# Kernel optimization log

Hardware: AMD Instinct MI355X
Metric: run time of the kernel (lower is better)

Reference implementation:

```python
import jax, jax.numpy as jnp
import numpy as np


def setup_inputs() -> dict:
    key = jax.random.key(0)
    k1, k2, k3, k4, k5 = jax.random.split(key, 5)
    B, T, D, H = 128, 512, 128, 512
    x = jax.random.normal(k1, (B, T, D), dtype=jnp.float32)
    h = jnp.zeros((B, H), dtype=jnp.float32)
    # tau in [1, 2) so the Euler step h + (-h + upd)/tau is stable
    tau = jax.random.uniform(k2, (B, 1), dtype=jnp.float32) + 1.0
    s_in = 1.0 / np.sqrt(D)
    s_rec = 1.0 / np.sqrt(H)
    # torch nn.Linear default init: U(-1/sqrt(fan_in), 1/sqrt(fan_in))
    W_in_w = jax.random.uniform(k3, (H, D), dtype=jnp.float32, minval=-s_in, maxval=s_in)
    W_in_b = jax.random.uniform(k4, (H,), dtype=jnp.float32, minval=-s_in, maxval=s_in)
    W_rec_w = jax.random.uniform(k5, (H, H), dtype=jnp.float32, minval=-s_rec, maxval=s_rec)
    return {"x": x, "h": h, "tau": tau, "W_in_w": W_in_w, "W_in_b": W_in_b, "W_rec_w": W_rec_w}


def reference(x, h, tau, W_in_w, W_in_b, W_rec_w):
    # Precompute the input projection for all timesteps in one big GEMM.
    # x: [B,T,D], W_in_w: [H,D] -> x_in: [B,T,H]
    x_in = jnp.einsum('btd,hd->bth', x, W_in_w) + W_in_b

    def step(h_t, xin_t):
        # xin_t: [B,H]; recurrent GEMM + tanh + Euler update (true data dep on h_t)
        upd = jnp.tanh(xin_t + h_t @ W_rec_w.T)
        h_new = h_t + (-h_t + upd) / tau
        return h_new, h_new

    h_last, h_seq = jax.lax.scan(step, h, jnp.swapaxes(x_in, 0, 1))  # scan over T
    return jnp.swapaxes(h_seq, 0, 1), h_last  # ([B,T,H], [B,H])
```

## Files before the change

### kernel.cpp

```cpp
#include <hip/hip_runtime.h>

#define B_SZ 128
#define T_SZ 512
#define D_SZ 128
#define H_SZ 512

#define NG 8
#define GB 16
#define NS 4
#define SN 128

typedef _Float16 f16;
typedef _Float16 f16x8 __attribute__((ext_vector_type(8)));
typedef _Float16 f16x4 __attribute__((ext_vector_type(4)));
typedef float f32x4 __attribute__((ext_vector_type(4)));
typedef unsigned long long ull;

__global__ __launch_bounds__(256) void transpose_k(const float* __restrict__ in,
                                                   float* __restrict__ out,
                                                   int R, int C) {
  __shared__ float tile[32][33];
  int c0 = blockIdx.x * 32, r0 = blockIdx.y * 32;
  int tx = threadIdx.x & 31, ty = threadIdx.x >> 5;
  for (int i = ty; i < 32; i += 8)
    tile[i][tx] = in[(size_t)(r0 + i) * C + (c0 + tx)];
  __syncthreads();
  for (int i = ty; i < 32; i += 8)
    out[(size_t)(c0 + i) * R + (r0 + tx)] = tile[tx][i];
}

__global__ __launch_bounds__(256) void input_proj_k(
    const float* __restrict__ x,
    const float* __restrict__ WTin,
    const float* __restrict__ bias,
    float* __restrict__ out)
{
  __shared__ float xs[32 * 128];
  const int tid = threadIdx.x;
  const size_t r0 = (size_t)blockIdx.x * 32;

  const float4* xg = (const float4*)(x + r0 * D_SZ);
  float4* xs4s = (float4*)xs;
#pragma unroll
  for (int i = 0; i < 4; ++i) xs4s[tid + i * 256] = xg[tid + i * 256];
  __syncthreads();

  const int q = tid & 127;
  const int rg = tid >> 7;
  const float4* W4 = (const float4*)WTin;
  const float4* xs4 = (const float4*)xs;

  float acc[16][4];
#pragma unroll
  for (int r = 0; r < 16; ++r)
#pragma unroll
    for (int c = 0; c < 4; ++c) acc[r][c] = 0.f;

  for (int k4 = 0; k4 < 32; ++k4) {
    float w[4][4];
#pragma unroll
    for (int kk = 0; kk < 4; ++kk) {
      float4 wv = W4[(size_t)(k4 * 4 + kk) * 128 + q];
      w[kk][0] = wv.x; w[kk][1] = wv.y; w[kk][2] = wv.z; w[kk][3] = wv.w;
    }
#pragma unroll
    for (int r = 0; r < 16; ++r) {
      float4 xv = xs4[(rg * 16 + r) * 32 + k4];
      float xk[4] = {xv.x, xv.y, xv.z, xv.w};
#pragma unroll
      for (int kk = 0; kk < 4; ++kk)
#pragma unroll
        for (int c = 0; c < 4; ++c)
          acc[r][c] = fmaf(xk[kk], w[kk][c], acc[r][c]);
    }
  }

  float4 bv = ((const float4*)bias)[q];
  float bb[4] = {bv.x, bv.y, bv.z, bv.w};
#pragma unroll
  for (int r = 0; r < 16; ++r) {
    float4 o;
    o.x = acc[r][0] + bb[0];
    o.y = acc[r][1] + bb[1];
    o.z = acc[r][2] + bb[2];
    o.w = acc[r][3] + bb[3];
    ((float4*)(out + (r0 + rg * 16 + r) * H_SZ))[q] = o;
  }
}

__device__ __forceinline__ float fast_tanh(float y) {
  float e = __expf(2.0f * y);
  return 1.0f - __fdividef(2.0f, e + 1.0f);
}

__device__ __forceinline__ ull ld_agent(const ull* p) {
  return __hip_atomic_load(p, __ATOMIC_RELAXED, __HIP_MEMORY_SCOPE_AGENT);
}

__global__ __launch_bounds__(512) void ltc_rec_mfma(
    float* __restrict__ seq,
    float* __restrict__ h_last,
    const float* __restrict__ hin,
    const float* __restrict__ tau,
    const float* __restrict__ Wrec,
    f16* __restrict__ ex)
{
  __shared__ f16 hs[2][GB * H_SZ];

  const int tid = threadIdx.x;
  const int g = blockIdx.x & 7;
  const int slice = blockIdx.x >> 3;
  const int w = tid >> 6;
  const int l = tid & 63;
  const int m = l & 15;
  const int kg = l >> 4;
  const int jt = slice * SN + w * 16;
  const int j0 = jt + kg * 4;
  const int b = g * GB + m;

  f16x8 afrag[16];
  {
    const float* wr = Wrec + (size_t)(jt + m) * H_SZ;
#pragma unroll
    for (int ff = 0; ff < 16; ++ff) {
      const int f = (slice * 4 + ff) & 15;
      const int k0 = f * 32 + kg * 8;
      float4 u0 = *(const float4*)(wr + k0);
      float4 u1 = *(const float4*)(wr + k0 + 4);
      f16x8 a;
      a[0] = (f16)u0.x; a[1] = (f16)u0.y; a[2] = (f16)u0.z; a[3] = (f16)u0.w;
      a[4] = (f16)u1.x; a[5] = (f16)u1.y; a[6] = (f16)u1.z; a[7] = (f16)u1.w;
      afrag[ff] = a;
    }
  }

  float hreg[4];
  {
    float4 h0 = *(const float4*)(hin + (size_t)b * H_SZ + j0);
    hreg[0] = h0.x; hreg[1] = h0.y; hreg[2] = h0.z; hreg[3] = h0.w;
  }
  const float itau = 1.0f / tau[b];

  {
    const int mr = tid >> 5;
    const int c4 = (tid & 31) * 4;
#pragma unroll
    for (int p = 0; p < 4; ++p) {
      const int col = p * SN + c4;
      float4 v = *(const float4*)(hin + (size_t)(g * GB + mr) * H_SZ + col);
      const int e = (mr * H_SZ + col) ^ ((mr & 7) << 3);
      f16x4 hf;
      hf[0] = (f16)v.x; hf[1] = (f16)v.y; hf[2] = (f16)v.z; hf[3] = (f16)v.w;
      *(f16x4*)&hs[0][e] = hf;
    }
  }
  __syncthreads();

  const size_t EXB = (size_t)GB * SN;
  const size_t RING_ULL = (size_t)NG * NS * EXB / 4;
  ull* pub0 = (ull*)(ex + ((size_t)g * NS + slice) * EXB + (size_t)m * SN + (w * 16 + kg * 4));

  const int gmr = tid >> 5;
  const int gc4 = (tid & 31) * 4;
  const int psa = (slice + 1) & 3, psb = (slice + 2) & 3, psc = (slice + 3) & 3;
  const ull* ga0 = (const ull*)(ex + ((size_t)g * NS + psa) * EXB + (size_t)gmr * SN + gc4);
  const ull* gb0 = (const ull*)(ex + ((size_t)g * NS + psb) * EXB + (size_t)gmr * SN + gc4);
  const ull* gc0 = (const ull*)(ex + ((size_t)g * NS + psc) * EXB + (size_t)gmr * SN + gc4);
  const int ea = (gmr * H_SZ + psa * SN + gc4) ^ ((gmr & 7) << 3);
  const int eb = (gmr * H_SZ + psb * SN + gc4) ^ ((gmr & 7) << 3);
  const int ec = (gmr * H_SZ + psc * SN + gc4) ^ ((gmr & 7) << 3);
  const int eown = (m * H_SZ + j0) ^ ((m & 7) << 3);

  int ebase[16];
#pragma unroll
  for (int ff = 0; ff < 16; ++ff) {
    const int f = (slice * 4 + ff) & 15;
    ebase[ff] = (m * H_SZ + f * 32 + kg * 8) ^ ((m & 7) << 3);
  }

  float* seqp = seq + (size_t)b * T_SZ * H_SZ + j0;
  float4 xin = *(const float4*)seqp;

  for (int s = 0; s < T_SZ; ++s) {
    const int cur = s & 1, nxt = cur ^ 1;

    ull w0 = 0, w1 = 0, w2 = 0;
    const size_t proff = nxt ? RING_ULL : 0;
    const ull ptag = (ull)(((s - 1) >> 1) & 1);
    if (s > 0) {
      w0 = ld_agent(ga0 + proff);
      w1 = ld_agent(gb0 + proff);
      w2 = ld_agent(gc0 + proff);
    }

    f32x4 accA = {0.f, 0.f, 0.f, 0.f};
    accA = __builtin_amdgcn_mfma_f32_16x16x32_f16(afrag[0], *(const f16x8*)&hs[cur][ebase[0]], accA, 0, 0, 0);
    accA = __builtin_amdgcn_mfma_f32_16x16x32_f16(afrag[1], *(const f16x8*)&hs[cur][ebase[1]], accA, 0, 0, 0);
    accA = __builtin_amdgcn_mfma_f32_16x16x32_f16(afrag[2], *(const f16x8*)&hs[cur][ebase[2]], accA, 0, 0, 0);
    accA = __builtin_amdgcn_mfma_f32_16x16x32_f16(afrag[3], *(const f16x8*)&hs[cur][ebase[3]], accA, 0, 0, 0);

    if (s > 0) {
      while ((w0 & 1ULL) != ptag) w0 = ld_agent(ga0 + proff);
      while ((w1 & 1ULL) != ptag) w1 = ld_agent(gb0 + proff);
      while ((w2 & 1ULL) != ptag) w2 = ld_agent(gc0 + proff);
      *(f16x4*)&hs[cur][ea] = __builtin_bit_cast(f16x4, w0);
      *(f16x4*)&hs[cur][eb] = __builtin_bit_cast(f16x4, w1);
      *(f16x4*)&hs[cur][ec] = __builtin_bit_cast(f16x4, w2);
      __syncthreads();
    }

    f32x4 accB = {0.f, 0.f, 0.f, 0.f};
    f32x4 accC = {0.f, 0.f, 0.f, 0.f};
    accB = __builtin_amdgcn_mfma_f32_16x16x32_f16(afrag[4],  *(const f16x8*)&hs[cur][ebase[4]],  accB, 0, 0, 0);
    accB = __builtin_amdgcn_mfma_f32_16x16x32_f16(afrag[5],  *(const f16x8*)&hs[cur][ebase[5]],  accB, 0, 0, 0);
    accB = __builtin_amdgcn_mfma_f32_16x16x32_f16(afrag[6],  *(const f16x8*)&hs[cur][ebase[6]],  accB, 0, 0, 0);
    accB = __builtin_amdgcn_mfma_f32_16x16x32_f16(afrag[7],  *(const f16x8*)&hs[cur][ebase[7]],  accB, 0, 0, 0);
    accB = __builtin_amdgcn_mfma_f32_16x16x32_f16(afrag[8],  *(const f16x8*)&hs[cur][ebase[8]],  accB, 0, 0, 0);
    accB = __builtin_amdgcn_mfma_f32_16x16x32_f16(afrag[9],  *(const f16x8*)&hs[cur][ebase[9]],  accB, 0, 0, 0);
    accC = __builtin_amdgcn_mfma_f32_16x16x32_f16(afrag[10], *(const f16x8*)&hs[cur][ebase[10]], accC, 0, 0, 0);
    accC = __builtin_amdgcn_mfma_f32_16x16x32_f16(afrag[11], *(const f16x8*)&hs[cur][ebase[11]], accC, 0, 0, 0);
    accC = __builtin_amdgcn_mfma_f32_16x16x32_f16(afrag[12], *(const f16x8*)&hs[cur][ebase[12]], accC, 0, 0, 0);
    accC = __builtin_amdgcn_mfma_f32_16x16x32_f16(afrag[13], *(const f16x8*)&hs[cur][ebase[13]], accC, 0, 0, 0);
    accC = __builtin_amdgcn_mfma_f32_16x16x32_f16(afrag[14], *(const f16x8*)&hs[cur][ebase[14]], accC, 0, 0, 0);
    accC = __builtin_amdgcn_mfma_f32_16x16x32_f16(afrag[15], *(const f16x8*)&hs[cur][ebase[15]], accC, 0, 0, 0);
    f32x4 acc = accA + accB + accC;

    float4 hv;
    hv.x = fmaf(fast_tanh(xin.x + acc[0]) - hreg[0], itau, hreg[0]);
    hv.y = fmaf(fast_tanh(xin.y + acc[1]) - hreg[1], itau, hreg[1]);
    hv.z = fmaf(fast_tanh(xin.z + acc[2]) - hreg[2], itau, hreg[2]);
    hv.w = fmaf(fast_tanh(xin.w + acc[3]) - hreg[3], itau, hreg[3]);
    hreg[0] = hv.x; hreg[1] = hv.y; hreg[2] = hv.z; hreg[3] = hv.w;

    f16x4 hf;
    hf[0] = (f16)hv.x; hf[1] = (f16)hv.y; hf[2] = (f16)hv.z; hf[3] = (f16)hv.w;

    {
      ull bits = __builtin_bit_cast(ull, hf);
      bits = (bits & ~1ULL) | (ull)((s >> 1) & 1);
      __hip_atomic_store(pub0 + (cur ? RING_ULL : 0), bits,
                         __ATOMIC_RELAXED, __HIP_MEMORY_SCOPE_AGENT);
    }

    *(f16x4*)&hs[nxt][eown] = hf;
    *(float4*)seqp = hv;
    seqp += H_SZ;
    xin = *(const float4*)seqp;

    __syncthreads();
  }

  float4 hv;
  hv.x = hreg[0]; hv.y = hreg[1]; hv.z = hreg[2]; hv.w = hreg[3];
  *(float4*)(h_last + (size_t)b * H_SZ + j0) = hv;
}

extern "C" void kernel_launch(void* const* d_in, const int* in_sizes, int n_in,
                              void* d_out, int out_size, void* d_ws, size_t ws_size,
                              hipStream_t stream) {
  const float* x     = (const float*)d_in[0];
  const float* hin   = (const float*)d_in[1];
  const float* tau   = (const float*)d_in[2];
  const float* Win_w = (const float*)d_in[3];
  const float* Win_b = (const float*)d_in[4];
  const float* Wrec  = (const float*)d_in[5];

  float* out    = (float*)d_out;
  float* seq    = out;
  float* h_last = out + (size_t)B_SZ * T_SZ * H_SZ;

  f16*   ex   = (f16*)d_ws;
  float* WTin = (float*)((char*)d_ws + 262144);

  hipMemsetAsync(ex, 0xFF, 2 * NG * NS * GB * SN * sizeof(f16), stream);

  dim3 blk(256);
  transpose_k<<<dim3(D_SZ / 32, H_SZ / 32), blk, 0, stream>>>(Win_w, WTin, H_SZ, D_SZ);
  input_proj_k<<<(B_SZ * T_SZ) / 32, blk, 0, stream>>>(x, WTin, Win_b, seq);
  ltc_rec_mfma<<<NG * NS, 512, 0, stream>>>(seq, h_last, hin, tau, Wrec, ex);
}
```

Before: 1.030 ms.

## Use MFMA for input projection and prefetch peer hidden-state exchange loads

```diff
diff --git a/kernel.cpp b/kernel.cpp
--- a/kernel.cpp
+++ b/kernel.cpp
@@ -9,82 +9,86 @@
 #define GB 16
 #define NS 4
 #define SN 128
+#define EXB (GB * SN)
+#define RING_ULL 16384
 
 typedef _Float16 f16;
 typedef _Float16 f16x8 __attribute__((ext_vector_type(8)));
 typedef _Float16 f16x4 __attribute__((ext_vector_type(4)));
 typedef float f32x4 __attribute__((ext_vector_type(4)));
 typedef unsigned long long ull;
-
-__global__ __launch_bounds__(256) void transpose_k(const float* __restrict__ in,
-                                                   float* __restrict__ out,
-                                                   int R, int C) {
-  __shared__ float tile[32][33];
-  int c0 = blockIdx.x * 32, r0 = blockIdx.y * 32;
-  int tx = threadIdx.x & 31, ty = threadIdx.x >> 5;
-  for (int i = ty; i < 32; i += 8)
-    tile[i][tx] = in[(size_t)(r0 + i) * C + (c0 + tx)];
-  __syncthreads();
-  for (int i = ty; i < 32; i += 8)
-    out[(size_t)(c0 + i) * R + (r0 + tx)] = tile[tx][i];
-}
-
-__global__ __launch_bounds__(256) void input_proj_k(
+typedef unsigned long long ull2 __attribute__((ext_vector_type(2)));
+typedef unsigned int uint;
+
+#define BAR()                                              \
+  do {                                                     \
+    asm volatile("s_waitcnt lgkmcnt(0)" ::: "memory");     \
+    __builtin_amdgcn_sched_barrier(0);                     \
+    __builtin_amdgcn_s_barrier();                          \
+    __builtin_amdgcn_sched_barrier(0);                     \
+  } while (0)
+
+__global__ __launch_bounds__(256) void input_proj_mfma(
     const float* __restrict__ x,
-    const float* __restrict__ WTin,
+    const float* __restrict__ Win,
     const float* __restrict__ bias,
     float* __restrict__ out)
 {
-  __shared__ float xs[32 * 128];
   const int tid = threadIdx.x;
-  const size_t r0 = (size_t)blockIdx.x * 32;
-
-  const float4* xg = (const float4*)(x + r0 * D_SZ);
-  float4* xs4s = (float4*)xs;
-#pragma unroll
-  for (int i = 0; i < 4; ++i) xs4s[tid + i * 256] = xg[tid + i * 256];
-  __syncthreads();
-
-  const int q = tid & 127;
-  const int rg = tid >> 7;
-  const float4* W4 = (const float4*)WTin;
-  const float4* xs4 = (const float4*)xs;
-
-  float acc[16][4];
-#pragma unroll
-  for (int r = 0; r < 16; ++r)
-#pragma unroll
-    for (int c = 0; c < 4; ++c) acc[r][c] = 0.f;
-
-  for (int k4 = 0; k4 < 32; ++k4) {
-    float w[4][4];
-#pragma unroll
-    for (int kk = 0; kk < 4; ++kk) {
-      float4 wv = W4[(size_t)(k4 * 4 + kk) * 128 + q];
-      w[kk][0] = wv.x; w[kk][1] = wv.y; w[kk][2] = wv.z; w[kk][3] = wv.w;
-    }
-#pragma unroll
-    for (int r = 0; r < 16; ++r) {
-      float4 xv = xs4[(rg * 16 + r) * 32 + k4];
-      float xk[4] = {xv.x, xv.y, xv.z, xv.w};
-#pragma unroll
-      for (int kk = 0; kk < 4; ++kk)
-#pragma unroll
-        for (int c = 0; c < 4; ++c)
-          acc[r][c] = fmaf(xk[kk], w[kk][c], acc[r][c]);
-    }
-  }
-
-  float4 bv = ((const float4*)bias)[q];
-  float bb[4] = {bv.x, bv.y, bv.z, bv.w};
-#pragma unroll
-  for (int r = 0; r < 16; ++r) {
-    float4 o;
-    o.x = acc[r][0] + bb[0];
-    o.y = acc[r][1] + bb[1];
-    o.z = acc[r][2] + bb[2];
-    o.w = acc[r][3] + bb[3];
-    ((float4*)(out + (r0 + rg * 16 + r) * H_SZ))[q] = o;
+  const int w = tid >> 6;
+  const int l = tid & 63;
+  const int m = l & 15;
+  const int kg = l >> 4;
+  const int ht = w * 128;
+
+  f16x8 af[8][4];
+#pragma unroll
+  for (int t = 0; t < 8; ++t) {
+    const float* wr = Win + (size_t)(ht + t * 16 + m) * D_SZ;
+#pragma unroll
+    for (int kb = 0; kb < 4; ++kb) {
+      const int k0 = kb * 32 + kg * 8;
+      float4 u0 = *(const float4*)(wr + k0);
+      float4 u1 = *(const float4*)(wr + k0 + 4);
+      f16x8 a;
+      a[0] = (f16)u0.x; a[1] = (f16)u0.y; a[2] = (f16)u0.z; a[3] = (f16)u0.w;
+      a[4] = (f16)u1.x; a[5] = (f16)u1.y; a[6] = (f16)u1.z; a[7] = (f16)u1.w;
+      af[t][kb] = a;
+    }
+  }
+
+  for (int rt = 0; rt < 8; ++rt) {
+    const size_t r0 = ((size_t)blockIdx.x * 8 + rt) * 16;
+    const float* xr = x + (r0 + m) * D_SZ + kg * 8;
+    f16x8 bf[4];
+#pragma unroll
+    for (int kb = 0; kb < 4; ++kb) {
+      float4 u0 = *(const float4*)(xr + kb * 32);
+      float4 u1 = *(const float4*)(xr + kb * 32 + 4);
+      f16x8 a;
+      a[0] = (f16)u0.x; a[1] = (f16)u0.y; a[2] = (f16)u0.z; a[3] = (f16)u0.w;
+      a[4] = (f16)u1.x; a[5] = (f16)u1.y; a[6] = (f16)u1.z; a[7] = (f16)u1.w;
+      bf[kb] = a;
+    }
+    f32x4 acc[8];
+#pragma unroll
+    for (int t = 0; t < 8; ++t) acc[t] = (f32x4){0.f, 0.f, 0.f, 0.f};
+#pragma unroll
+    for (int kb = 0; kb < 4; ++kb)
+#pragma unroll
+      for (int t = 0; t < 8; ++t)
+        acc[t] = __builtin_amdgcn_mfma_f32_16x16x32_f16(af[t][kb], bf[kb], acc[t], 0, 0, 0);
+#pragma unroll
+    for (int t = 0; t < 8; ++t) {
+      const int c0 = ht + t * 16 + kg * 4;
+      float4 bb = *(const float4*)(bias + c0);
+      float4 o;
+      o.x = acc[t][0] + bb.x;
+      o.y = acc[t][1] + bb.y;
+      o.z = acc[t][2] + bb.z;
+      o.w = acc[t][3] + bb.w;
+      *(float4*)(out + (r0 + m) * H_SZ + c0) = o;
+    }
   }
 }
 
@@ -103,9 +107,9 @@
     const float* __restrict__ hin,
     const float* __restrict__ tau,
     const float* __restrict__ Wrec,
-    f16* __restrict__ ex)
+    ull* __restrict__ exu)
 {
-  __shared__ f16 hs[2][GB * H_SZ];
+  __shared__ __attribute__((aligned(16))) f16 hs[2][GB * H_SZ];
 
   const int tid = threadIdx.x;
   const int g = blockIdx.x & 7;
@@ -117,6 +121,7 @@
   const int jt = slice * SN + w * 16;
   const int j0 = jt + kg * 4;
   const int b = g * GB + m;
+  const int msk = (m & 7) << 3;
 
   f16x8 afrag[16];
   {
@@ -156,42 +161,34 @@
   }
   __syncthreads();
 
-  const size_t EXB = (size_t)GB * SN;
-  const size_t RING_ULL = (size_t)NG * NS * EXB / 4;
-  ull* pub0 = (ull*)(ex + ((size_t)g * NS + slice) * EXB + (size_t)m * SN + (w * 16 + kg * 4));
-
-  const int gmr = tid >> 5;
-  const int gc4 = (tid & 31) * 4;
-  const int psa = (slice + 1) & 3, psb = (slice + 2) & 3, psc = (slice + 3) & 3;
-  const ull* ga0 = (const ull*)(ex + ((size_t)g * NS + psa) * EXB + (size_t)gmr * SN + gc4);
-  const ull* gb0 = (const ull*)(ex + ((size_t)g * NS + psb) * EXB + (size_t)gmr * SN + gc4);
-  const ull* gc0 = (const ull*)(ex + ((size_t)g * NS + psc) * EXB + (size_t)gmr * SN + gc4);
-  const int ea = (gmr * H_SZ + psa * SN + gc4) ^ ((gmr & 7) << 3);
-  const int eb = (gmr * H_SZ + psb * SN + gc4) ^ ((gmr & 7) << 3);
-  const int ec = (gmr * H_SZ + psc * SN + gc4) ^ ((gmr & 7) << 3);
-  const int eown = (m * H_SZ + j0) ^ ((m & 7) << 3);
+  const uint pidx = (uint)((g * 4 + slice) * 512 + m * 32 + w * 4 + kg);
+
+  const int qA = tid & 255, pnoA = tid >> 8;
+  const int psA = (slice + 1 + pnoA) & 3;
+  const int rowA = qA >> 4, cA = qA & 15;
+  const uint gA = (uint)((g * 4 + psA) * 512 + rowA * 32 + cA * 2);
+  const int eA = (rowA * H_SZ + psA * SN + cA * 8) ^ ((rowA & 7) << 3);
+
+  const int psB = (slice + 3) & 3;
+  const int rowB = qA >> 4, cB = qA & 15;
+  const uint gB = (uint)((g * 4 + psB) * 512 + rowB * 32 + cB * 2);
+  const int eB = (rowB * H_SZ + psB * SN + cB * 8) ^ ((rowB & 7) << 3);
 
   int ebase[16];
 #pragma unroll
   for (int ff = 0; ff < 16; ++ff) {
     const int f = (slice * 4 + ff) & 15;
-    ebase[ff] = (m * H_SZ + f * 32 + kg * 8) ^ ((m & 7) << 3);
-  }
+    ebase[ff] = (m * H_SZ + f * 32 + kg * 8) ^ msk;
+  }
+  const int eown = (m * H_SZ + j0) ^ msk;
 
   float* seqp = seq + (size_t)b * T_SZ * H_SZ + j0;
   float4 xin = *(const float4*)seqp;
 
+  ull gwA0 = 0, gwA1 = 0, gwB0 = 0, gwB1 = 0;
+
   for (int s = 0; s < T_SZ; ++s) {
     const int cur = s & 1, nxt = cur ^ 1;
-
-    ull w0 = 0, w1 = 0, w2 = 0;
-    const size_t proff = nxt ? RING_ULL : 0;
-    const ull ptag = (ull)(((s - 1) >> 1) & 1);
-    if (s > 0) {
-      w0 = ld_agent(ga0 + proff);
-      w1 = ld_agent(gb0 + proff);
-      w2 = ld_agent(gc0 + proff);
-    }
 
     f32x4 accA = {0.f, 0.f, 0.f, 0.f};
     accA = __builtin_amdgcn_mfma_f32_16x16x32_f16(afrag[0], *(const f16x8*)&hs[cur][ebase[0]], accA, 0, 0, 0);
@@ -200,14 +197,22 @@
     accA = __builtin_amdgcn_mfma_f32_16x16x32_f16(afrag[3], *(const f16x8*)&hs[cur][ebase[3]], accA, 0, 0, 0);
 
     if (s > 0) {
-      while ((w0 & 1ULL) != ptag) w0 = ld_agent(ga0 + proff);
-      while ((w1 & 1ULL) != ptag) w1 = ld_agent(gb0 + proff);
-      while ((w2 & 1ULL) != ptag) w2 = ld_agent(gc0 + proff);
-      *(f16x4*)&hs[cur][ea] = __builtin_bit_cast(f16x4, w0);
-      *(f16x4*)&hs[cur][eb] = __builtin_bit_cast(f16x4, w1);
-      *(f16x4*)&hs[cur][ec] = __builtin_bit_cast(f16x4, w2);
-      __syncthreads();
-    }
+      const ull vtag = (ull)(((s - 1) >> 1) & 1);
+      const uint voff = ((s - 1) & 1) ? (uint)RING_ULL : 0u;
+      while ((gwA0 & 1ULL) != vtag) gwA0 = ld_agent(exu + voff + gA);
+      while ((gwA1 & 1ULL) != vtag) gwA1 = ld_agent(exu + voff + gA + 1);
+      {
+        ull2 t; t[0] = gwA0; t[1] = gwA1;
+        *(ull2*)&hs[cur][eA] = t;
+      }
+      if (tid < 256) {
+        while ((gwB0 & 1ULL) != vtag) gwB0 = ld_agent(exu + voff + gB);
+        while ((gwB1 & 1ULL) != vtag) gwB1 = ld_agent(exu + voff + gB + 1);
+        ull2 t; t[0] = gwB0; t[1] = gwB1;
+        *(ull2*)&hs[cur][eB] = t;
+      }
+    }
+    BAR();
 
     f32x4 accB = {0.f, 0.f, 0.f, 0.f};
     f32x4 accC = {0.f, 0.f, 0.f, 0.f};
@@ -235,11 +240,17 @@
     f16x4 hf;
     hf[0] = (f16)hv.x; hf[1] = (f16)hv.y; hf[2] = (f16)hv.z; hf[3] = (f16)hv.w;
 
+    const uint ioff = cur ? (uint)RING_ULL : 0u;
     {
-      ull bits = __builtin_bit_cast(ull, hf);
-      bits = (bits & ~1ULL) | (ull)((s >> 1) & 1);
-      __hip_atomic_store(pub0 + (cur ? RING_ULL : 0), bits,
-                         __ATOMIC_RELAXED, __HIP_MEMORY_SCOPE_AGENT);
+      ull bits = (__builtin_bit_cast(ull, hf) & ~1ULL) | (ull)((s >> 1) & 1);
+      __hip_atomic_store(exu + ioff + pidx, bits, __ATOMIC_RELAXED, __HIP_MEMORY_SCOPE_AGENT);
+    }
+
+    gwA0 = ld_agent(exu + ioff + gA);
+    gwA1 = ld_agent(exu + ioff + gA + 1);
+    if (tid < 256) {
+      gwB0 = ld_agent(exu + ioff + gB);
+      gwB1 = ld_agent(exu + ioff + gB + 1);
     }
 
     *(f16x4*)&hs[nxt][eown] = hf;
@@ -247,7 +258,7 @@
     seqp += H_SZ;
     xin = *(const float4*)seqp;
 
-    __syncthreads();
+    BAR();
   }
 
   float4 hv;
@@ -269,13 +280,10 @@
   float* seq    = out;
   float* h_last = out + (size_t)B_SZ * T_SZ * H_SZ;
 
-  f16*   ex   = (f16*)d_ws;
-  float* WTin = (float*)((char*)d_ws + 262144);
+  ull* ex = (ull*)d_ws;
 
   hipMemsetAsync(ex, 0xFF, 2 * NG * NS * GB * SN * sizeof(f16), stream);
 
-  dim3 blk(256);
-  transpose_k<<<dim3(D_SZ / 32, H_SZ / 32), blk, 0, stream>>>(Win_w, WTin, H_SZ, D_SZ);
-  input_proj_k<<<(B_SZ * T_SZ) / 32, blk, 0, stream>>>(x, WTin, Win_b, seq);
+  input_proj_mfma<<<512, 256, 0, stream>>>(x, Win_w, Win_b, seq);
   ltc_rec_mfma<<<NG * NS, 512, 0, stream>>>(seq, h_last, hin, tau, Wrec, ex);
 }
```

Result: slower. 1.597 ms (+55.1%).
